# Kernel tuning notes

Measured on AMD Instinct MI355X. Metric: run time of the kernel, lower is better.

The kernel has to match this reference:

```python
import jax, jax.numpy as jnp
import numpy as np

N = 8192        # n_nodes == in_features (forced by elementwise input * W)
F_OUT = 128     # out_features
ALPHA = 0.2     # LeakyReLU negative slope
NEG_BIG = -9.0e15


def setup_inputs() -> dict:
    key = jax.random.key(0)
    k1, k2, k3, k4, k5 = jax.random.split(key, 5)
    x = jax.random.normal(k1, (N, F_OUT), dtype=jnp.float32)
    adj = jax.random.randint(k2, (N, N), 0, 2, dtype=jnp.int32)
    # xavier_uniform-style params
    W = jax.random.uniform(k3, (N, F_OUT), dtype=jnp.float32, minval=-1.0, maxval=1.0) * np.float32(1.414 * np.sqrt(6.0 / (N + F_OUT)))
    a = jax.random.uniform(k4, (2 * F_OUT, 1), dtype=jnp.float32, minval=-1.0, maxval=1.0) * np.float32(1.414 * np.sqrt(6.0 / (2 * F_OUT + 1)))
    W2 = jax.random.uniform(k5, (N, 1), dtype=jnp.float32, minval=-1.0, maxval=1.0) * np.float32(1.414 * np.sqrt(6.0 / (N + 1)))
    return {"x": x, "adj": adj, "W": W, "a": a, "W2": W2}


def reference(x, adj, W, a, W2):
    # h = input * W  (elementwise, shapes [N, F])
    h = x * W
    f = W.shape[1]
    # e[i,j] = leakyrelu( concat(h[i], h[j]) @ a ) = leakyrelu(h[i]@a1 + h[j]@a2)
    f1 = h @ a[:f]        # [N, 1]
    f2 = h @ a[f:]        # [N, 1]
    e = jax.nn.leaky_relu(f1 + f2.T, negative_slope=ALPHA)  # [N, N]
    e = jnp.where(adj > 0, e, NEG_BIG)
    attention = jax.nn.softmax(e, axis=1)  # dropout rate = 0.0 -> no-op
    h_prime = attention @ h                # [N, F] (stored as side effect in original)
    # output path: elu( (adj @ W2).T @ x ).T  -> [F, 1]
    adj_f = adj.astype(x.dtype)
    h_prime_3 = ((adj_f @ W2).T @ x).T     # [F, 1]
    out = jax.nn.elu(h_prime_3)            # concat=True branch
    return out, h_prime
```

## Files before the change

kernel.cpp:

```cpp
#include <hip/hip_runtime.h>
#include <hip/hip_bf16.h>

#define ALPHA 0.2f

typedef __attribute__((ext_vector_type(8)))  __bf16 bf16x8;
typedef __attribute__((ext_vector_type(16))) float  f32x16;
typedef int          i32x4 __attribute__((ext_vector_type(4)));
typedef float        f32x4 __attribute__((ext_vector_type(4)));
typedef unsigned int u32x4 __attribute__((ext_vector_type(4)));

static __device__ __forceinline__ unsigned short bf16bits(float v) {
    __bf16 b = (__bf16)v;
    unsigned short u;
    __builtin_memcpy(&u, &b, 2);
    return u;
}

__global__ __launch_bounds__(256) void gat_prep(
    const float* __restrict__ x, const float* __restrict__ W, const float* __restrict__ a,
    float* __restrict__ f1, float* __restrict__ f2, unsigned short* __restrict__ hB,
    float* __restrict__ ws_acc)
{
    __shared__ unsigned short lh[32][136];
    int t = threadIdx.x;
    int i0 = blockIdx.x * 32;
    if (blockIdx.x == 0 && t < 128) ws_acc[t] = 0.0f;

    int row = t >> 3, q = t & 7;
    int i = i0 + row;
    const float4* xp  = (const float4*)(x + (size_t)i * 128 + q * 16);
    const float4* wp  = (const float4*)(W + (size_t)i * 128 + q * 16);
    const float4* a1p = (const float4*)(a + q * 16);
    const float4* a2p = (const float4*)(a + 128 + q * 16);
    float p1 = 0.f, p2 = 0.f;
    #pragma unroll
    for (int jj = 0; jj < 4; ++jj) {
        float4 xv = xp[jj], wv = wp[jj], a1v = a1p[jj], a2v = a2p[jj];
        float h0 = xv.x * wv.x, h1 = xv.y * wv.y, h2 = xv.z * wv.z, h3 = xv.w * wv.w;
        p1 += h0 * a1v.x + h1 * a1v.y + h2 * a1v.z + h3 * a1v.w;
        p2 += h0 * a2v.x + h1 * a2v.y + h2 * a2v.z + h3 * a2v.w;
        int fb = q * 16 + jj * 4;
        lh[row][fb + 0] = bf16bits(h0);
        lh[row][fb + 1] = bf16bits(h1);
        lh[row][fb + 2] = bf16bits(h2);
        lh[row][fb + 3] = bf16bits(h3);
    }
    p1 += __shfl_xor(p1, 1); p1 += __shfl_xor(p1, 2); p1 += __shfl_xor(p1, 4);
    p2 += __shfl_xor(p2, 1); p2 += __shfl_xor(p2, 2); p2 += __shfl_xor(p2, 4);
    if (q == 0) { f1[i] = p1; f2[i] = p2; }
    __syncthreads();

    int fl = t >> 5, s0 = t & 31;
    int ksl = fl >> 2, ft = fl & 3;
    size_t fragbase = ((size_t)(2 * blockIdx.x + ksl) * 4 + ft) * 512;
    #pragma unroll
    for (int hw = 0; hw < 2; ++hw) {
        int s = s0 + hw * 32;
        int jl = ksl * 16 + hw * 8;
        int f = ft * 32 + s0;
        unsigned int p[4];
        #pragma unroll
        for (int k = 0; k < 4; ++k) {
            unsigned int lo = lh[jl + 2 * k][f];
            unsigned int hi = lh[jl + 2 * k + 1][f];
            p[k] = lo | (hi << 16);
        }
        u32x4 v = {p[0], p[1], p[2], p[3]};
        *(u32x4*)(hB + fragbase + s * 8) = v;
    }
}

__global__ __launch_bounds__(512, 2) void gat_main(
    const int* __restrict__ adj, const float* __restrict__ x,
    const float* __restrict__ W2, const float* __restrict__ f1g,
    const float* __restrict__ f2g, const unsigned short* __restrict__ hB,
    float* __restrict__ hp, float* __restrict__ ws_acc)
{
    __shared__ unsigned short wtile[32][1040];
    __shared__ float den_s[32], rs_s[32];

    int tid = threadIdx.x;
    int wv = tid >> 6, l = tid & 63;
    int r0 = wv * 4;
    int ft = wv & 3, jh = wv >> 2;
    int i0 = blockIdx.x * 32;

    float f1r[4];
    #pragma unroll
    for (int ri = 0; ri < 4; ++ri) f1r[ri] = f1g[i0 + r0 + ri];

    f32x16 acc = {};
    float den4[4] = {0.f, 0.f, 0.f, 0.f}, rs4[4] = {0.f, 0.f, 0.f, 0.f};

    const int* abase = adj + (size_t)(i0 + r0) * 8192 + l * 4;

    i32x4 adjreg[4][4];
    f32x4 f2reg[4], w2reg[4];
    auto issue = [&](int c) {
        int j0 = c << 10;
        #pragma unroll
        for (int js = 0; js < 4; ++js) {
            int jo = j0 + js * 256 + l * 4;
            f2reg[js] = *(const f32x4*)(f2g + jo);
            w2reg[js] = *(const f32x4*)(W2 + jo);
            #pragma unroll
            for (int ri = 0; ri < 4; ++ri)
                adjreg[ri][js] = __builtin_nontemporal_load(
                    (const i32x4*)(abase + (size_t)ri * 8192 + j0 + js * 256));
        }
    };
    issue(0);

    for (int c = 0; c < 8; ++c) {
        #pragma unroll
        for (int js = 0; js < 4; ++js) {
            f32x4 f2v = f2reg[js], w2v = w2reg[js];
            #pragma unroll
            for (int ri = 0; ri < 4; ++ri) {
                i32x4 ad = adjreg[ri][js];
                float wg[4];
                float rsum = 0.f, dsum = 0.f;
                #pragma unroll
                for (int e = 0; e < 4; ++e) {
                    float tt = f1r[ri] + f2v[e];
                    float lr = fmaxf(tt, ALPHA * tt);
                    float ex = __expf(lr);
                    float g = (ad[e] != 0) ? ex : 0.0f;
                    wg[e] = g;
                    dsum += g;
                    rsum += (ad[e] != 0) ? w2v[e] : 0.0f;
                }
                den4[ri] += dsum;
                rs4[ri] += rsum;
                unsigned int p0 = bf16bits(wg[0]) | ((unsigned int)bf16bits(wg[1]) << 16);
                unsigned int p1 = bf16bits(wg[2]) | ((unsigned int)bf16bits(wg[3]) << 16);
                *(uint2*)&wtile[r0 + ri][js * 256 + l * 4] = make_uint2(p0, p1);
            }
        }
        __syncthreads();
        if (c < 7) issue(c + 1);

        const unsigned short* wrow = &wtile[l & 31][(jh << 9) + ((l >> 5) << 3)];
        const unsigned short* bptr = hB + (((size_t)(c * 64 + jh * 32) * 4 + ft) << 9) + (l << 3);
        #pragma unroll
        for (int ksl = 0; ksl < 32; ++ksl) {
            bf16x8 afrag = *(const bf16x8*)(wrow + ksl * 16);
            bf16x8 bfrag = *(const bf16x8*)(bptr + (size_t)ksl * 2048);
            acc = __builtin_amdgcn_mfma_f32_32x32x16_bf16(afrag, bfrag, acc, 0, 0, 0);
        }
        __syncthreads();
    }

    #pragma unroll
    for (int ri = 0; ri < 4; ++ri) {
        float d = den4[ri], r = rs4[ri];
        #pragma unroll
        for (int off = 1; off < 64; off <<= 1) {
            d += __shfl_xor(d, off);
            r += __shfl_xor(r, off);
        }
        if (l == 0) { den_s[r0 + ri] = d; rs_s[r0 + ri] = r; }
    }

    float* buf = (float*)&wtile[0][0];
    float* av = (float*)&acc;
    if (jh == 1) {
        #pragma unroll
        for (int j = 0; j < 16; ++j) buf[ft * 1024 + j * 64 + l] = av[j];
    }
    __syncthreads();
    if (jh == 0) {
        #pragma unroll
        for (int j = 0; j < 16; ++j) av[j] += buf[ft * 1024 + j * 64 + l];
        #pragma unroll
        for (int reg = 0; reg < 16; ++reg) {
            int rrow = (reg & 3) + 8 * (reg >> 2) + 4 * (l >> 5);
            float dr = den_s[rrow];
            float rv = (dr != 0.f) ? av[reg] / dr : 0.f;
            __builtin_nontemporal_store(rv,
                hp + (size_t)(i0 + rrow) * 128 + ft * 32 + (l & 31));
        }
    }

    if (wv == 0) {
        float px = 0.f, py = 0.f;
        #pragma unroll 4
        for (int mm = 0; mm < 32; ++mm) {
            float rm = rs_s[mm];
            const float* xr = x + (size_t)(i0 + mm) * 128;
            px += rm * xr[l];
            py += rm * xr[l + 64];
        }
        atomicAdd(ws_acc + l, px);
        atomicAdd(ws_acc + l + 64, py);
    }
}

__global__ __launch_bounds__(128) void gat_finish(const float* __restrict__ ws_acc,
                                                  float* __restrict__ out)
{
    int t = threadIdx.x;
    float v = ws_acc[t];
    out[t] = (v > 0.f) ? v : (__expf(v) - 1.0f);
}

extern "C" void kernel_launch(void* const* d_in, const int* in_sizes, int n_in,
                              void* d_out, int out_size, void* d_ws, size_t ws_size,
                              hipStream_t stream) {
    const float* x   = (const float*)d_in[0];
    const int*   adj = (const int*)d_in[1];
    const float* W   = (const float*)d_in[2];
    const float* a   = (const float*)d_in[3];
    const float* W2  = (const float*)d_in[4];
    float* out = (float*)d_out;

    float* wsf    = (float*)d_ws;
    float* ws_acc = wsf;
    float* f1     = wsf + 128;
    float* f2     = wsf + 128 + 8192;
    unsigned short* hB = (unsigned short*)(wsf + 128 + 2 * 8192);

    gat_prep<<<256, 256, 0, stream>>>(x, W, a, f1, f2, hB, ws_acc);
    gat_main<<<256, 512, 0, stream>>>(adj, x, W2, f1, f2, hB, out + 128, ws_acc);
    gat_finish<<<1, 128, 0, stream>>>(ws_acc, out);
}
```

Baseline: 435.1 us.

## Warp-specialize GAT main kernel into producer/MFMA consumer waves with double-buffered tile

Splits each block into four producer waves that compute masked exp attention weights into a double-buffered LDS tile and four consumer waves that run 16x16x32 bf16 MFMAs on the previous chunk. Block rows drop from 32 to 16 and the grid doubles to 512 blocks with a higher occupancy target. The hB fragment layout in the prep kernel is reordered to match the new MFMA shape. The aim is to overlap the adjacency streaming and exp work with matrix math and to raise occupancy. The cost is that hB is read twice as many times overall and only half the waves issue adj loads.

```diff
diff --git a/kernel.cpp b/kernel.cpp
--- a/kernel.cpp
+++ b/kernel.cpp
@@ -4,7 +4,6 @@
 #define ALPHA 0.2f
 
 typedef __attribute__((ext_vector_type(8)))  __bf16 bf16x8;
-typedef __attribute__((ext_vector_type(16))) float  f32x16;
 typedef int          i32x4 __attribute__((ext_vector_type(4)));
 typedef float        f32x4 __attribute__((ext_vector_type(4)));
 typedef unsigned int u32x4 __attribute__((ext_vector_type(4)));
@@ -50,14 +49,13 @@
     if (q == 0) { f1[i] = p1; f2[i] = p2; }
     __syncthreads();
 
-    int fl = t >> 5, s0 = t & 31;
-    int ksl = fl >> 2, ft = fl & 3;
-    size_t fragbase = ((size_t)(2 * blockIdx.x + ksl) * 4 + ft) * 512;
+    int ftl = t >> 5, s0 = t & 31;
+    size_t fragbase = ((size_t)blockIdx.x * 8 + ftl) * 512;
     #pragma unroll
     for (int hw = 0; hw < 2; ++hw) {
         int s = s0 + hw * 32;
-        int jl = ksl * 16 + hw * 8;
-        int f = ft * 32 + s0;
+        int jl = (s >> 4) * 8;
+        int f = ftl * 16 + (s & 15);
         unsigned int p[4];
         #pragma unroll
         for (int k = 0; k < 4; ++k) {
@@ -70,36 +68,40 @@
     }
 }
 
-__global__ __launch_bounds__(512, 2) void gat_main(
+__global__ __launch_bounds__(512, 4) void gat_main(
     const int* __restrict__ adj, const float* __restrict__ x,
     const float* __restrict__ W2, const float* __restrict__ f1g,
     const float* __restrict__ f2g, const unsigned short* __restrict__ hB,
     float* __restrict__ hp, float* __restrict__ ws_acc)
 {
-    __shared__ unsigned short wtile[32][1040];
-    __shared__ float den_s[32], rs_s[32];
+    __shared__ unsigned short wtile[2][16][536];
+    __shared__ float den_s[16], rs_s[16];
 
     int tid = threadIdx.x;
     int wv = tid >> 6, l = tid & 63;
-    int r0 = wv * 4;
-    int ft = wv & 3, jh = wv >> 2;
-    int i0 = blockIdx.x * 32;
-
-    float f1r[4];
-    #pragma unroll
-    for (int ri = 0; ri < 4; ++ri) f1r[ri] = f1g[i0 + r0 + ri];
-
-    f32x16 acc = {};
+    int i0 = blockIdx.x * 16;
+    bool producer = (wv < 4);
+    int pw = wv & 3;
+    int r0 = pw * 4;
+    int tf0 = (wv & 3) * 2;
+
+    float f1r[4] = {0.f, 0.f, 0.f, 0.f};
     float den4[4] = {0.f, 0.f, 0.f, 0.f}, rs4[4] = {0.f, 0.f, 0.f, 0.f};
-
-    const int* abase = adj + (size_t)(i0 + r0) * 8192 + l * 4;
-
-    i32x4 adjreg[4][4];
-    f32x4 f2reg[4], w2reg[4];
+    i32x4 adjreg[4][2];
+    f32x4 f2reg[2], w2reg[2];
+    const int* abase = adj;
+    f32x4 acc0 = {}, acc1 = {};
+
+    if (producer) {
+        #pragma unroll
+        for (int ri = 0; ri < 4; ++ri) f1r[ri] = f1g[i0 + r0 + ri];
+        abase = adj + (size_t)(i0 + r0) * 8192 + l * 4;
+    }
+
     auto issue = [&](int c) {
-        int j0 = c << 10;
-        #pragma unroll
-        for (int js = 0; js < 4; ++js) {
+        int j0 = c << 9;
+        #pragma unroll
+        for (int js = 0; js < 2; ++js) {
             int jo = j0 + js * 256 + l * 4;
             f2reg[js] = *(const f32x4*)(f2g + jo);
             w2reg[js] = *(const f32x4*)(W2 + jo);
@@ -109,83 +111,86 @@
                     (const i32x4*)(abase + (size_t)ri * 8192 + j0 + js * 256));
         }
     };
-    issue(0);
-
-    for (int c = 0; c < 8; ++c) {
-        #pragma unroll
-        for (int js = 0; js < 4; ++js) {
-            f32x4 f2v = f2reg[js], w2v = w2reg[js];
-            #pragma unroll
-            for (int ri = 0; ri < 4; ++ri) {
-                i32x4 ad = adjreg[ri][js];
-                float wg[4];
-                float rsum = 0.f, dsum = 0.f;
+
+    if (producer) issue(0);
+
+    for (int c = 0; c <= 16; ++c) {
+        if (producer) {
+            if (c < 16) {
+                int buf = c & 1;
                 #pragma unroll
-                for (int e = 0; e < 4; ++e) {
-                    float tt = f1r[ri] + f2v[e];
-                    float lr = fmaxf(tt, ALPHA * tt);
-                    float ex = __expf(lr);
-                    float g = (ad[e] != 0) ? ex : 0.0f;
-                    wg[e] = g;
-                    dsum += g;
-                    rsum += (ad[e] != 0) ? w2v[e] : 0.0f;
+                for (int js = 0; js < 2; ++js) {
+                    f32x4 f2v = f2reg[js], w2v = w2reg[js];
+                    #pragma unroll
+                    for (int ri = 0; ri < 4; ++ri) {
+                        i32x4 ad = adjreg[ri][js];
+                        float wg[4];
+                        float dsum = 0.f, rsum = 0.f;
+                        #pragma unroll
+                        for (int e = 0; e < 4; ++e) {
+                            float tt = f1r[ri] + f2v[e];
+                            float lr = fmaxf(tt, ALPHA * tt);
+                            float ex = __expf(lr);
+                            float g = (ad[e] != 0) ? ex : 0.0f;
+                            wg[e] = g;
+                            dsum += g;
+                            rsum += (ad[e] != 0) ? w2v[e] : 0.0f;
+                        }
+                        den4[ri] += dsum;
+                        rs4[ri] += rsum;
+                        unsigned int p0 = bf16bits(wg[0]) | ((unsigned int)bf16bits(wg[1]) << 16);
+                        unsigned int p1 = bf16bits(wg[2]) | ((unsigned int)bf16bits(wg[3]) << 16);
+                        *(uint2*)&wtile[buf][r0 + ri][js * 256 + l * 4] = make_uint2(p0, p1);
+                    }
                 }
-                den4[ri] += dsum;
-                rs4[ri] += rsum;
-                unsigned int p0 = bf16bits(wg[0]) | ((unsigned int)bf16bits(wg[1]) << 16);
-                unsigned int p1 = bf16bits(wg[2]) | ((unsigned int)bf16bits(wg[3]) << 16);
-                *(uint2*)&wtile[r0 + ri][js * 256 + l * 4] = make_uint2(p0, p1);
+                if (c < 15) issue(c + 1);
+            } else {
+                #pragma unroll
+                for (int ri = 0; ri < 4; ++ri) {
+                    float d = den4[ri], r = rs4[ri];
+                    #pragma unroll
+                    for (int off = 1; off < 64; off <<= 1) {
+                        d += __shfl_xor(d, off);
+                        r += __shfl_xor(r, off);
+                    }
+                    if (l == 0) { den_s[r0 + ri] = d; rs_s[r0 + ri] = r; }
+                }
             }
+        } else {
+            if (c > 0) {
+                int cc = c - 1;
+                int buf = cc & 1;
+                const unsigned short* ar = &wtile[buf][l & 15][(l >> 4) * 8];
+                const unsigned short* bp = hB + (((size_t)cc * 16) * 8 + tf0) * 512 + l * 8;
+                #pragma unroll
+                for (int ks = 0; ks < 16; ++ks) {
+                    bf16x8 af = *(const bf16x8*)(ar + ks * 32);
+                    bf16x8 b0 = *(const bf16x8*)(bp + (size_t)ks * 4096);
+                    bf16x8 b1 = *(const bf16x8*)(bp + (size_t)ks * 4096 + 512);
+                    acc0 = __builtin_amdgcn_mfma_f32_16x16x32_bf16(af, b0, acc0, 0, 0, 0);
+                    acc1 = __builtin_amdgcn_mfma_f32_16x16x32_bf16(af, b1, acc1, 0, 0, 0);
+                }
+            }
         }
         __syncthreads();
-        if (c < 7) issue(c + 1);
-
-        const unsigned short* wrow = &wtile[l & 31][(jh << 9) + ((l >> 5) << 3)];
-        const unsigned short* bptr = hB + (((size_t)(c * 64 + jh * 32) * 4 + ft) << 9) + (l << 3);
-        #pragma unroll
-        for (int ksl = 0; ksl < 32; ++ksl) {
-            bf16x8 afrag = *(const bf16x8*)(wrow + ksl * 16);
-            bf16x8 bfrag = *(const bf16x8*)(bptr + (size_t)ksl * 2048);
-            acc = __builtin_amdgcn_mfma_f32_32x32x16_bf16(afrag, bfrag, acc, 0, 0, 0);
-        }
-        __syncthreads();
-    }
-
-    #pragma unroll
-    for (int ri = 0; ri < 4; ++ri) {
-        float d = den4[ri], r = rs4[ri];
-        #pragma unroll
-        for (int off = 1; off < 64; off <<= 1) {
-            d += __shfl_xor(d, off);
-            r += __shfl_xor(r, off);
-        }
-        if (l == 0) { den_s[r0 + ri] = d; rs_s[r0 + ri] = r; }
-    }
-
-    float* buf = (float*)&wtile[0][0];
-    float* av = (float*)&acc;
-    if (jh == 1) {
-        #pragma unroll
-        for (int j = 0; j < 16; ++j) buf[ft * 1024 + j * 64 + l] = av[j];
-    }
-    __syncthreads();
-    if (jh == 0) {
-        #pragma unroll
-        for (int j = 0; j < 16; ++j) av[j] += buf[ft * 1024 + j * 64 + l];
-        #pragma unroll
-        for (int reg = 0; reg < 16; ++reg) {
-            int rrow = (reg & 3) + 8 * (reg >> 2) + 4 * (l >> 5);
-            float dr = den_s[rrow];
-            float rv = (dr != 0.f) ? av[reg] / dr : 0.f;
-            __builtin_nontemporal_store(rv,
-                hp + (size_t)(i0 + rrow) * 128 + ft * 32 + (l & 31));
-        }
-    }
-
-    if (wv == 0) {
+    }
+
+    if (!producer) {
+        int col = l & 15, rq = l >> 4;
+        #pragma unroll
+        for (int reg = 0; reg < 4; ++reg) {
+            int row = rq * 4 + reg;
+            float dr = den_s[row];
+            float inv = (dr != 0.f) ? 1.0f / dr : 0.f;
+            __builtin_nontemporal_store(acc0[reg] * inv,
+                hp + (size_t)(i0 + row) * 128 + tf0 * 16 + col);
+            __builtin_nontemporal_store(acc1[reg] * inv,
+                hp + (size_t)(i0 + row) * 128 + tf0 * 16 + 16 + col);
+        }
+    } else if (wv == 0) {
         float px = 0.f, py = 0.f;
         #pragma unroll 4
-        for (int mm = 0; mm < 32; ++mm) {
+        for (int mm = 0; mm < 16; ++mm) {
             float rm = rs_s[mm];
             const float* xr = x + (size_t)(i0 + mm) * 128;
             px += rm * xr[l];
@@ -221,6 +226,6 @@
     unsigned short* hB = (unsigned short*)(wsf + 128 + 2 * 8192);
 
     gat_prep<<<256, 256, 0, stream>>>(x, W, a, f1, f2, hB, ws_acc);
-    gat_main<<<256, 512, 0, stream>>>(adj, x, W2, f1, f2, hB, out + 128, ws_acc);
+    gat_main<<<512, 512, 0, stream>>>(adj, x, W2, f1, f2, hB, out + 128, ws_acc);
     gat_finish<<<1, 128, 0, stream>>>(ws_acc, out);
 }
```

Result: slower. 450.9 us (+3.6%).

## Split K across waves with per-wave 16x16 MFMA tiles and no block barriers

Applied to the files above, without the earlier changes.

Each block now handles 16 rows with 4 waves. Each wave owns a disjoint quarter of the neighbor dimension and computes all 128 output features using 16x16x32 bf16 MFMAs from a private LDS tile. This removes the two block-wide __syncthreads per chunk. Partial accumulators, denominators and W2 row sums are reduced across waves at the end, and the hB fragment layout in prep is changed to match. Grid doubles to 512 blocks of 256 threads, trading higher register pressure (16 adj vectors, 8 accumulators) and more hB reads per row for less synchronization and more parallelism.

```diff
diff --git a/kernel.cpp b/kernel.cpp
--- a/kernel.cpp
+++ b/kernel.cpp
@@ -4,7 +4,6 @@
 #define ALPHA 0.2f
 
 typedef __attribute__((ext_vector_type(8)))  __bf16 bf16x8;
-typedef __attribute__((ext_vector_type(16))) float  f32x16;
 typedef int          i32x4 __attribute__((ext_vector_type(4)));
 typedef float        f32x4 __attribute__((ext_vector_type(4)));
 typedef unsigned int u32x4 __attribute__((ext_vector_type(4)));
@@ -50,14 +49,13 @@
     if (q == 0) { f1[i] = p1; f2[i] = p2; }
     __syncthreads();
 
-    int fl = t >> 5, s0 = t & 31;
-    int ksl = fl >> 2, ft = fl & 3;
-    size_t fragbase = ((size_t)(2 * blockIdx.x + ksl) * 4 + ft) * 512;
+    int ftl = t >> 5, s0 = t & 31;
+    size_t fragbase = ((size_t)blockIdx.x * 8 + ftl) * 512;
     #pragma unroll
     for (int hw = 0; hw < 2; ++hw) {
         int s = s0 + hw * 32;
-        int jl = ksl * 16 + hw * 8;
-        int f = ft * 32 + s0;
+        int jl = (s >> 4) * 8;
+        int f = ftl * 16 + (s & 15);
         unsigned int p[4];
         #pragma unroll
         for (int k = 0; k < 4; ++k) {
@@ -70,124 +68,134 @@
     }
 }
 
-__global__ __launch_bounds__(512, 2) void gat_main(
+__global__ __launch_bounds__(256, 2) void gat_main(
     const int* __restrict__ adj, const float* __restrict__ x,
     const float* __restrict__ W2, const float* __restrict__ f1g,
     const float* __restrict__ f2g, const unsigned short* __restrict__ hB,
     float* __restrict__ hp, float* __restrict__ ws_acc)
 {
-    __shared__ unsigned short wtile[32][1040];
-    __shared__ float den_s[32], rs_s[32];
+    __shared__ unsigned short tile[4][16][264];
+    __shared__ float den_s[4][16], rs_s[4][16];
 
     int tid = threadIdx.x;
-    int wv = tid >> 6, l = tid & 63;
-    int r0 = wv * 4;
-    int ft = wv & 3, jh = wv >> 2;
-    int i0 = blockIdx.x * 32;
-
-    float f1r[4];
-    #pragma unroll
-    for (int ri = 0; ri < 4; ++ri) f1r[ri] = f1g[i0 + r0 + ri];
-
-    f32x16 acc = {};
-    float den4[4] = {0.f, 0.f, 0.f, 0.f}, rs4[4] = {0.f, 0.f, 0.f, 0.f};
-
-    const int* abase = adj + (size_t)(i0 + r0) * 8192 + l * 4;
-
-    i32x4 adjreg[4][4];
-    f32x4 f2reg[4], w2reg[4];
+    int w = tid >> 6, l = tid & 63;
+    int i0 = blockIdx.x * 16;
+
+    float f1r[16];
+    #pragma unroll
+    for (int r = 0; r < 16; ++r) f1r[r] = f1g[i0 + r];
+
+    float den[16], rs[16];
+    #pragma unroll
+    for (int r = 0; r < 16; ++r) { den[r] = 0.f; rs[r] = 0.f; }
+    f32x4 acc[8] = {};
+
+    const int jbase0 = w * 2048;
+    const int* arow = adj + (size_t)i0 * 8192 + jbase0 + l * 4;
+    const float* f2p = f2g + jbase0 + l * 4;
+    const float* w2p = W2 + jbase0 + l * 4;
+
+    i32x4 adjreg[16];
+    f32x4 f2v, w2v;
     auto issue = [&](int c) {
-        int j0 = c << 10;
-        #pragma unroll
-        for (int js = 0; js < 4; ++js) {
-            int jo = j0 + js * 256 + l * 4;
-            f2reg[js] = *(const f32x4*)(f2g + jo);
-            w2reg[js] = *(const f32x4*)(W2 + jo);
-            #pragma unroll
-            for (int ri = 0; ri < 4; ++ri)
-                adjreg[ri][js] = __builtin_nontemporal_load(
-                    (const i32x4*)(abase + (size_t)ri * 8192 + j0 + js * 256));
-        }
+        int jo = c * 256;
+        f2v = *(const f32x4*)(f2p + jo);
+        w2v = *(const f32x4*)(w2p + jo);
+        #pragma unroll
+        for (int r = 0; r < 16; ++r)
+            adjreg[r] = __builtin_nontemporal_load(
+                (const i32x4*)(arow + (size_t)r * 8192 + jo));
     };
     issue(0);
 
+    const unsigned short* hBw = hB + (size_t)w * 262144 + l * 8;
+    const unsigned short* ap  = &tile[w][l & 15][(l >> 4) * 8];
+
     for (int c = 0; c < 8; ++c) {
         #pragma unroll
-        for (int js = 0; js < 4; ++js) {
-            f32x4 f2v = f2reg[js], w2v = w2reg[js];
-            #pragma unroll
-            for (int ri = 0; ri < 4; ++ri) {
-                i32x4 ad = adjreg[ri][js];
-                float wg[4];
-                float rsum = 0.f, dsum = 0.f;
-                #pragma unroll
-                for (int e = 0; e < 4; ++e) {
-                    float tt = f1r[ri] + f2v[e];
-                    float lr = fmaxf(tt, ALPHA * tt);
-                    float ex = __expf(lr);
-                    float g = (ad[e] != 0) ? ex : 0.0f;
-                    wg[e] = g;
-                    dsum += g;
-                    rsum += (ad[e] != 0) ? w2v[e] : 0.0f;
-                }
-                den4[ri] += dsum;
-                rs4[ri] += rsum;
-                unsigned int p0 = bf16bits(wg[0]) | ((unsigned int)bf16bits(wg[1]) << 16);
-                unsigned int p1 = bf16bits(wg[2]) | ((unsigned int)bf16bits(wg[3]) << 16);
-                *(uint2*)&wtile[r0 + ri][js * 256 + l * 4] = make_uint2(p0, p1);
+        for (int r = 0; r < 16; ++r) {
+            i32x4 ad = adjreg[r];
+            float g[4];
+            float dsum = 0.f, rsum = 0.f;
+            #pragma unroll
+            for (int e = 0; e < 4; ++e) {
+                float tt = f1r[r] + f2v[e];
+                float lr = fmaxf(tt, ALPHA * tt);
+                float ex = __expf(lr);
+                float gg = (ad[e] != 0) ? ex : 0.0f;
+                g[e] = gg;
+                dsum += gg;
+                rsum += (ad[e] != 0) ? w2v[e] : 0.0f;
             }
-        }
-        __syncthreads();
+            den[r] += dsum;
+            rs[r] += rsum;
+            unsigned int p0 = bf16bits(g[0]) | ((unsigned int)bf16bits(g[1]) << 16);
+            unsigned int p1 = bf16bits(g[2]) | ((unsigned int)bf16bits(g[3]) << 16);
+            *(uint2*)&tile[w][r][l * 4] = make_uint2(p0, p1);
+        }
         if (c < 7) issue(c + 1);
-
-        const unsigned short* wrow = &wtile[l & 31][(jh << 9) + ((l >> 5) << 3)];
-        const unsigned short* bptr = hB + (((size_t)(c * 64 + jh * 32) * 4 + ft) << 9) + (l << 3);
-        #pragma unroll
-        for (int ksl = 0; ksl < 32; ++ksl) {
-            bf16x8 afrag = *(const bf16x8*)(wrow + ksl * 16);
-            bf16x8 bfrag = *(const bf16x8*)(bptr + (size_t)ksl * 2048);
-            acc = __builtin_amdgcn_mfma_f32_32x32x16_bf16(afrag, bfrag, acc, 0, 0, 0);
-        }
-        __syncthreads();
-    }
-
-    #pragma unroll
-    for (int ri = 0; ri < 4; ++ri) {
-        float d = den4[ri], r = rs4[ri];
+        const unsigned short* bp = hBw + (size_t)c * 32768;
+        #pragma unroll
+        for (int ksl = 0; ksl < 8; ++ksl) {
+            bf16x8 af = *(const bf16x8*)(ap + ksl * 32);
+            const unsigned short* bk = bp + (size_t)ksl * 4096;
+            #pragma unroll
+            for (int ft = 0; ft < 8; ++ft) {
+                bf16x8 bf = *(const bf16x8*)(bk + ft * 512);
+                acc[ft] = __builtin_amdgcn_mfma_f32_16x16x32_bf16(af, bf, acc[ft], 0, 0, 0);
+            }
+        }
+    }
+
+    #pragma unroll
+    for (int r = 0; r < 16; ++r) {
+        float d = den[r], rr = rs[r];
         #pragma unroll
         for (int off = 1; off < 64; off <<= 1) {
             d += __shfl_xor(d, off);
-            r += __shfl_xor(r, off);
-        }
-        if (l == 0) { den_s[r0 + ri] = d; rs_s[r0 + ri] = r; }
-    }
-
-    float* buf = (float*)&wtile[0][0];
-    float* av = (float*)&acc;
-    if (jh == 1) {
-        #pragma unroll
-        for (int j = 0; j < 16; ++j) buf[ft * 1024 + j * 64 + l] = av[j];
+            rr += __shfl_xor(rr, off);
+        }
+        if (l == 0) { den_s[w][r] = d; rs_s[w][r] = rr; }
+    }
+
+    float* av = (float*)acc;
+    if (w != 0) {
+        float* dst = (float*)&tile[0][0][0] + (size_t)(w - 1) * 2048;
+        #pragma unroll
+        for (int j = 0; j < 32; ++j) dst[j * 64 + l] = av[j];
     }
     __syncthreads();
-    if (jh == 0) {
-        #pragma unroll
-        for (int j = 0; j < 16; ++j) av[j] += buf[ft * 1024 + j * 64 + l];
-        #pragma unroll
-        for (int reg = 0; reg < 16; ++reg) {
-            int rrow = (reg & 3) + 8 * (reg >> 2) + 4 * (l >> 5);
-            float dr = den_s[rrow];
-            float rv = (dr != 0.f) ? av[reg] / dr : 0.f;
-            __builtin_nontemporal_store(rv,
-                hp + (size_t)(i0 + rrow) * 128 + ft * 32 + (l & 31));
-        }
-    }
-
-    if (wv == 0) {
+
+    if (w == 0) {
+        #pragma unroll
+        for (int ww = 0; ww < 3; ++ww) {
+            const float* srcp = (const float*)&tile[0][0][0] + (size_t)ww * 2048;
+            #pragma unroll
+            for (int j = 0; j < 32; ++j) av[j] += srcp[j * 64 + l];
+        }
+        int q = l >> 4, col = l & 15;
+        float inv[4];
+        #pragma unroll
+        for (int reg = 0; reg < 4; ++reg) {
+            int row = q * 4 + reg;
+            float dsum = den_s[0][row] + den_s[1][row] + den_s[2][row] + den_s[3][row];
+            inv[reg] = (dsum != 0.f) ? 1.0f / dsum : 0.f;
+        }
+        #pragma unroll
+        for (int ft = 0; ft < 8; ++ft) {
+            #pragma unroll
+            for (int reg = 0; reg < 4; ++reg) {
+                int row = q * 4 + reg;
+                __builtin_nontemporal_store(acc[ft][reg] * inv[reg],
+                    hp + (size_t)(i0 + row) * 128 + ft * 16 + col);
+            }
+        }
+    } else if (w == 1) {
         float px = 0.f, py = 0.f;
-        #pragma unroll 4
-        for (int mm = 0; mm < 32; ++mm) {
-            float rm = rs_s[mm];
-            const float* xr = x + (size_t)(i0 + mm) * 128;
+        #pragma unroll
+        for (int r = 0; r < 16; ++r) {
+            float rm = rs_s[0][r] + rs_s[1][r] + rs_s[2][r] + rs_s[3][r];
+            const float* xr = x + (size_t)(i0 + r) * 128;
             px += rm * xr[l];
             py += rm * xr[l + 64];
         }
@@ -221,6 +229,6 @@
     unsigned short* hB = (unsigned short*)(wsf + 128 + 2 * 8192);
 
     gat_prep<<<256, 256, 0, stream>>>(x, W, a, f1, f2, hB, ws_acc);
-    gat_main<<<256, 512, 0, stream>>>(adj, x, W2, f1, f2, hB, out + 128, ws_acc);
+    gat_main<<<512, 256, 0, stream>>>(adj, x, W2, f1, f2, hB, out + 128, ws_acc);
     gat_finish<<<1, 128, 0, stream>>>(ws_acc, out);
 }
```

Result: slower. 487.7 us (+12.1%).
